# Kernel optimization log

Measured on AMD Instinct MI355X. Metric: run time of the kernel, lower is better.

Reference implementation:

```python
import jax, jax.numpy as jnp
import numpy as np

L, H, P = 16384, 1024, 512
DT_MIN, DT_MAX = 1e-3, 1e-1
STEP_RESCALE = 1.0


def setup_inputs() -> dict:
    key = jax.random.key(0)
    ks = jax.random.split(key, 7)
    input_sequence = jax.random.normal(ks[0], (L, H), jnp.float32)
    # eigenvalues with negative real part (left half plane), HiPPO-like imag parts
    Lambda_re = -(jax.random.uniform(ks[1], (P,), jnp.float32) * 0.9 + 0.1)
    Lambda_im = jnp.pi * jnp.arange(P, dtype=jnp.float32)
    B = jax.random.normal(ks[2], (P, H, 2), jnp.float32) / jnp.sqrt(2.0 * H)   # real/imag of B_tilde (P,H)
    C = jax.random.normal(ks[3], (H, P, 2), jnp.float32) / jnp.sqrt(2.0 * P)   # real/imag of C_tilde (H,P)
    D = jax.random.normal(ks[4], (H,), jnp.float32)
    u01 = jax.random.uniform(ks[5], (P, 1), jnp.float32)
    log_step = jnp.log(DT_MIN) + u01 * (jnp.log(DT_MAX) - jnp.log(DT_MIN))     # (P,1)
    return dict(input_sequence=input_sequence, Lambda_re=Lambda_re, Lambda_im=Lambda_im,
                B=B, C=C, D=D, log_step=log_step)


def _binop(q_i, q_j):
    # diagonal linear recurrence composition: (A, b) pairs
    A_i, b_i = q_i
    A_j, b_j = q_j
    return A_j * A_i, A_j * b_i + b_j


def reference(input_sequence, Lambda_re, Lambda_im, B, C, D, log_step):
    Lambda = Lambda_re + 1j * Lambda_im                        # (P,) complex64
    B_tilde = B[..., 0] + 1j * B[..., 1]                       # (P,H)
    C_tilde = C[..., 0] + 1j * C[..., 1]                       # (H,P)
    step = STEP_RESCALE * jnp.exp(log_step[:, 0])              # (P,)
    # ZOH discretization
    Lambda_bar = jnp.exp(Lambda * step)                        # (P,)
    B_bar = ((Lambda_bar - 1.0) / Lambda)[:, None] * B_tilde   # (P,H)
    # Bu_elements: (L,P) complex
    Bu = input_sequence.astype(B_bar.dtype) @ B_bar.T
    Lambda_elems = jnp.broadcast_to(Lambda_bar, Bu.shape)      # (L,P)
    # parallel associative scan over the diagonal recurrence x_t = Lambda_bar*x_{t-1} + Bu_t
    _, xs = jax.lax.associative_scan(_binop, (Lambda_elems, Bu))
    ys = 2.0 * (xs @ C_tilde.T).real                           # conj_sym => factor 2, (L,H)
    return ys + D * input_sequence
```

## Files before the change

### kernel.cpp

```cpp
#include <hip/hip_runtime.h>
#include <math.h>

#define L_SEQ 16384
#define H_DIM 1024
#define P_DIM 512
#define N2P   1024
#define KDIM  1024
#define NKT   16
#define CHUNK 64
#define NCHUNK 256

typedef __attribute__((ext_vector_type(8))) short short8;
typedef __attribute__((ext_vector_type(4))) float f32x4;
typedef __attribute__((address_space(3))) const char* lds3_t;

__device__ __forceinline__ unsigned short f2bf(float f){
    unsigned int u = __float_as_uint(f);
    u = (u + 0x7FFFu + ((u >> 16) & 1u)) >> 16;
    return (unsigned short)u;
}
__device__ __forceinline__ float bf2f(unsigned int lo16){
    return __uint_as_float(lo16 << 16);
}

__global__ void k_prep_lambda(const float* __restrict__ lre, const float* __restrict__ lim,
                              const float* __restrict__ lstep,
                              float* __restrict__ lam, float* __restrict__ coef,
                              float* __restrict__ lpow, float* __restrict__ wtab)
{
    int p = threadIdx.x;
    double step = exp((double)lstep[p]);
    double dr = (double)lre[p], di = (double)lim[p];
    double ar = dr*step, ai = di*step;
    double er = exp(ar);
    double lbr = er*cos(ai), lbi = er*sin(ai);
    lam[2*p] = (float)lbr; lam[2*p+1] = (float)lbi;
    double nr = lbr - 1.0, ni = lbi;
    double d2 = dr*dr + di*di;
    coef[2*p]   = (float)((nr*dr + ni*di)/d2);
    coef[2*p+1] = (float)((ni*dr - nr*di)/d2);
    double pwr = 1.0, pwi = 0.0;
    for (int tt = 63; tt >= 0; --tt){
        wtab[((size_t)tt*P_DIM + p)*2]     = (float)pwr;
        wtab[((size_t)tt*P_DIM + p)*2 + 1] = (float)pwi;
        double t2 = pwr*lbr - pwi*lbi;
        pwi = pwr*lbi + pwi*lbr;
        pwr = t2;
    }
    double xr = lbr, xi = lbi;
    #pragma unroll
    for (int s=0;s<6;s++){ double t = xr*xr - xi*xi; xi = 2.0*xr*xi; xr = t; }
    lpow[2*p] = (float)xr; lpow[2*p+1] = (float)xi;
}

__global__ __launch_bounds__(256)
void k_prep_misc(const float* __restrict__ B, const float* __restrict__ C,
                 const float* __restrict__ coef,
                 unsigned short* __restrict__ BB, unsigned short* __restrict__ CC,
                 const float4* __restrict__ u, unsigned short* __restrict__ u16)
{
    int bid = blockIdx.x;
    if (bid < 2048){
        int i = bid*256 + threadIdx.x;
        int p = i >> 10, h = i & 1023;
        float br = B[2*i], bi = B[2*i+1];
        float cr = coef[2*p], ci = coef[2*p+1];
        BB[(size_t)(2*p)*H_DIM + h]   = f2bf(cr*br - ci*bi);
        BB[(size_t)(2*p+1)*H_DIM + h] = f2bf(cr*bi + ci*br);
    } else if (bid < 4096){
        int i = (bid-2048)*256 + threadIdx.x;
        int h = i >> 9, p = i & 511;
        float cr = C[2*i], ci = C[2*i+1];
        CC[(size_t)h*N2P + 2*p]     = f2bf(2.f*cr);
        CC[(size_t)h*N2P + 2*p + 1] = f2bf(-2.f*ci);
    } else {
        int i = (bid-4096)*256 + threadIdx.x;
        float4 a = u[2*i], b = u[2*i+1];
        union { short8 v; unsigned short s[8]; } r;
        r.s[0]=f2bf(a.x); r.s[1]=f2bf(a.y); r.s[2]=f2bf(a.z); r.s[3]=f2bf(a.w);
        r.s[4]=f2bf(b.x); r.s[5]=f2bf(b.y); r.s[6]=f2bf(b.z); r.s[7]=f2bf(b.w);
        *reinterpret_cast<short8*>(u16 + (size_t)i*8) = r.v;
    }
}

template<int EPI>
__global__ __launch_bounds__(512, 2)
void gemm256(const unsigned short* __restrict__ A, const unsigned short* __restrict__ Bm,
             float* __restrict__ Cf, unsigned short* __restrict__ Cb,
             const float* __restrict__ Dv, const unsigned short* __restrict__ U16,
             const float* __restrict__ wtab, float* __restrict__ aggOut)
{
    __shared__ char lds[131072];
    const int tid  = threadIdx.x;
    const int lane = tid & 63;
    const int wid  = tid >> 6;
    const int wm = wid >> 2, wn = wid & 3;
    const int wg = ((int)blockIdx.x & 7) * 32 + ((int)blockIdx.x >> 3);
    const int tm = wg >> 2, tn = wg & 3;
    const int lr = lane & 15;

    const int scol = ((tid & 7) ^ ((tid >> 3) & 7)) << 3;
    const int srow = tid >> 3;
    const int kc0 = (((lane >> 4)      ^ (lr & 7)) << 4);
    const int kc1 = ((((lane >> 4) | 4) ^ (lr & 7)) << 4);
    const int aSub = wm*16384 + lr*128;
    const int bSub = 32768 + (wn >> 1)*16384 + (wn & 1)*8192 + lr*128;

#define GLOAD(SRC, DST) __builtin_amdgcn_global_load_lds( \
        (const __attribute__((address_space(1))) void*)(SRC), \
        (__attribute__((address_space(3))) void*)(DST), 16, 0, 0)
#define STAGE_A(src_, par_, h_) do{ \
    char* d_ = lds + ((par_)<<16) + (h_)*16384 + tid*16; \
    const unsigned short* s_ = A + (size_t)(tm*256 + (h_)*128 + srow)*KDIM + (size_t)(src_)*64 + scol; \
    GLOAD(s_, d_); GLOAD(s_ + (size_t)64*KDIM, d_ + 8192); }while(0)
#define STAGE_B(src_, par_, h_) do{ \
    char* d_ = lds + ((par_)<<16) + 32768 + (h_)*16384 + tid*16; \
    const unsigned short* s_ = Bm + (size_t)(tn*256 + (h_)*128 + srow)*KDIM + (size_t)(src_)*64 + scol; \
    GLOAD(s_, d_); GLOAD(s_ + (size_t)64*KDIM, d_ + 8192); }while(0)
#define DSR(D, P, IMM) asm volatile("ds_read_b128 %0, %1 offset:" IMM : "=v"(D) : "v"(P))
#define LGKM(N) do{ asm volatile("s_waitcnt lgkmcnt(" #N ")" ::: "memory"); \
                    __builtin_amdgcn_sched_barrier(0); }while(0)
#define VMC0  asm volatile("s_waitcnt vmcnt(0)" ::: "memory")
#define ABAR  asm volatile("s_barrier" ::: "memory")
#define SB0   __builtin_amdgcn_sched_barrier(0)
#define MFMA(a,b,c) __builtin_amdgcn_mfma_f32_16x16x32_bf16(a,b,c,0,0,0)
#define PRIO1 __builtin_amdgcn_s_setprio(1)
#define PRIO0 __builtin_amdgcn_s_setprio(0)

    short8 a1[4], a2[4], bb0[4], bb1[4];
    f32x4 acc[8][4];
    #pragma unroll
    for (int m=0;m<8;m++)
        #pragma unroll
        for (int n=0;n<4;n++) acc[m][n] = (f32x4){0.f,0.f,0.f,0.f};

    STAGE_A(0,0,0); STAGE_A(0,0,1); STAGE_B(0,0,0); STAGE_B(0,0,1);
    VMC0; ABAR;

    #pragma unroll 2
    for (int kt = 0; kt < NKT; ++kt) {
        const int sb   = (kt & 1) << 16;
        const int dpar = (~kt) & 1;
        const int src  = (kt+1 < NKT) ? kt+1 : NKT-1;
        lds3_t pa0 = (lds3_t)(lds + sb + aSub + kc0);
        lds3_t pa1 = (lds3_t)(lds + sb + aSub + kc1);
        lds3_t pb0 = (lds3_t)(lds + sb + bSub + kc0);
        lds3_t pb1 = (lds3_t)(lds + sb + bSub + kc1);

        DSR(a1[0], pa0, "0");    DSR(a1[1], pa0, "2048");
        DSR(a1[2], pa0, "4096"); DSR(a1[3], pa0, "6144");
        DSR(bb0[0], pb0, "0");    DSR(bb0[1], pb0, "2048");
        DSR(bb0[2], pb0, "4096"); DSR(bb0[3], pb0, "6144");
        STAGE_A(src, dpar, 0); STAGE_A(src, dpar, 1);
        DSR(a2[0], pa0, "8192");  DSR(a2[1], pa0, "10240");
        DSR(a2[2], pa0, "12288"); DSR(a2[3], pa0, "14336");
        LGKM(4);
        PRIO1;
        #pragma unroll
        for (int m=0;m<4;m++)
            #pragma unroll
            for (int n=0;n<4;n++) acc[m][n] = MFMA(a1[m], bb0[n], acc[m][n]);
        PRIO0; SB0;
        DSR(a1[0], pa1, "0");    DSR(a1[1], pa1, "2048");
        DSR(a1[2], pa1, "4096"); DSR(a1[3], pa1, "6144");
        DSR(bb1[0], pb1, "0");    DSR(bb1[1], pb1, "2048");
        DSR(bb1[2], pb1, "4096"); DSR(bb1[3], pb1, "6144");
        STAGE_B(src, dpar, 0); STAGE_B(src, dpar, 1);
        LGKM(8);
        PRIO1;
        #pragma unroll
        for (int m=0;m<4;m++)
            #pragma unroll
            for (int n=0;n<4;n++) acc[4+m][n] = MFMA(a2[m], bb0[n], acc[4+m][n]);
        PRIO0; SB0;
        DSR(a2[0], pa1, "8192");  DSR(a2[1], pa1, "10240");
        DSR(a2[2], pa1, "12288"); DSR(a2[3], pa1, "14336");
        LGKM(4);
        PRIO1;
        #pragma unroll
        for (int m=0;m<4;m++)
            #pragma unroll
            for (int n=0;n<4;n++) acc[m][n] = MFMA(a1[m], bb1[n], acc[m][n]);
        PRIO0; SB0;
        LGKM(0);
        PRIO1;
        #pragma unroll
        for (int m=0;m<4;m++)
            #pragma unroll
            for (int n=0;n<4;n++) acc[4+m][n] = MFMA(a2[m], bb1[n], acc[4+m][n]);
        PRIO0; SB0;
        VMC0;
        ABAR;
    }

    if (!EPI){
        const int q = lane >> 4;
        #pragma unroll
        for (int n=0;n<4;n++){
            const int pg = tn*128 + wn*32 + n*8 + (lr >> 1);
            float wr[16], wi[16];
            #pragma unroll
            for (int mm=0;mm<4;mm++)
                #pragma unroll
                for (int j=0;j<4;j++){
                    const float* wp = wtab + ((size_t)(mm*16 + q*4 + j)*P_DIM + pg)*2;
                    wr[mm*4+j] = wp[0]; wi[mm*4+j] = wp[1];
                }
            #pragma unroll
            for (int h=0; h<2; h++){
                float s1 = 0.f, s2 = 0.f;
                #pragma unroll
                for (int mm=0;mm<4;mm++)
                    #pragma unroll
                    for (int j=0;j<4;j++){
                        float x = acc[h*4+mm][n][j];
                        s1 += wr[mm*4+j]*x;
                        s2 += wi[mm*4+j]*x;
                    }
                s1 += __shfl_xor(s1,16); s1 += __shfl_xor(s1,32);
                s2 += __shfl_xor(s2,16); s2 += __shfl_xor(s2,32);
                float s1p = __shfl_xor(s1,1);
                float s2p = __shfl_xor(s2,1);
                if (lane < 16 && !(lr & 1)){
                    int c = 4*tm + 2*wm + h;
                    float* o = aggOut + ((size_t)c*P_DIM + pg)*2;
                    o[0] = s1 - s2p;
                    o[1] = s2 + s1p;
                }
            }
        }
    }

    const int orow0 = tm*256 + wm*128 + (lane>>4)*4;
    const int ocol0 = tn*256 + wn*64 + lr;
    #pragma unroll
    for (int m=0;m<8;m++){
        #pragma unroll
        for (int n=0;n<4;n++){
            int row = orow0 + m*16, col = ocol0 + n*16;
            #pragma unroll
            for (int j=0;j<4;j++){
                size_t idx = (size_t)(row + j)*N2P + col;
                if (EPI) Cf[idx] = acc[m][n][j] + Dv[col]*bf2f(U16[idx]);
                else     Cb[idx] = f2bf(acc[m][n][j]);
            }
        }
    }
#undef GLOAD
#undef STAGE_A
#undef STAGE_B
#undef DSR
#undef LGKM
#undef VMC0
#undef ABAR
#undef SB0
#undef MFMA
#undef PRIO1
#undef PRIO0
}

__global__ __launch_bounds__(256)
void k_scan(float* __restrict__ agg, const float* __restrict__ lpow)
{
    __shared__ float sr[NCHUNK], si[NCHUNK];
    int c = threadIdx.x, p = blockIdx.x;
    float xr = agg[((size_t)c*P_DIM + p)*2];
    float xi = agg[((size_t)c*P_DIM + p)*2 + 1];
    sr[c] = xr; si[c] = xi;
    float wr = lpow[2*p], wi = lpow[2*p+1];
    for (int s=1; s<NCHUNK; s<<=1){
        __syncthreads();
        float ur = 0.f, ui = 0.f;
        if (c >= s){ ur = sr[c-s]; ui = si[c-s]; }
        __syncthreads();
        xr += wr*ur - wi*ui;
        xi += wr*ui + wi*ur;
        sr[c] = xr; si[c] = xi;
        float t = wr*wr - wi*wi; wi = 2.f*wr*wi; wr = t;
    }
    __syncthreads();
    float er = 0.f, ei = 0.f;
    if (c > 0){ er = sr[c-1]; ei = si[c-1]; }
    agg[((size_t)c*P_DIM + p)*2]     = er;
    agg[((size_t)c*P_DIM + p)*2 + 1] = ei;
}

__global__ __launch_bounds__(512)
void k_apply(const unsigned int* __restrict__ Bu, const float* __restrict__ lam,
             const float* __restrict__ xinit, unsigned int* __restrict__ xs)
{
    int p = threadIdx.x, c = blockIdx.x;
    float lrr = lam[2*p], lii = lam[2*p+1];
    float xr = xinit[((size_t)c*P_DIM + p)*2];
    float xi = xinit[((size_t)c*P_DIM + p)*2 + 1];
    const unsigned int* b2 = Bu + (size_t)c*CHUNK*512 + p;
    unsigned int* o = xs + (size_t)c*CHUNK*512 + p;
    #pragma unroll 4
    for (int t=0;t<CHUNK;t++){
        unsigned int b = b2[(size_t)t*512];
        float br = __uint_as_float(b << 16);
        float bi = __uint_as_float(b & 0xffff0000u);
        float tr = lrr*xr - lii*xi + br;
        xi = lrr*xi + lii*xr + bi;
        xr = tr;
        o[(size_t)t*512] = (unsigned int)f2bf(xr) | ((unsigned int)f2bf(xi) << 16);
    }
}

extern "C" void kernel_launch(void* const* d_in, const int* in_sizes, int n_in,
                              void* d_out, int out_size, void* d_ws, size_t ws_size,
                              hipStream_t stream)
{
    const float* u   = (const float*)d_in[0];
    const float* lre = (const float*)d_in[1];
    const float* lim = (const float*)d_in[2];
    const float* B   = (const float*)d_in[3];
    const float* C   = (const float*)d_in[4];
    const float* D   = (const float*)d_in[5];
    const float* ls  = (const float*)d_in[6];
    float* out = (float*)d_out;

    char* w = (char*)d_ws;
    unsigned short* u16  = (unsigned short*)(w + 0);
    unsigned short* xs16 = (unsigned short*)(w + 33554432);
    unsigned short* Bu16 = (unsigned short*)(w + 67108864);
    unsigned short* BB   = (unsigned short*)(w + 100663296);
    unsigned short* CC   = (unsigned short*)(w + 102760448);
    float* lam   = (float*)(w + 104857600);
    float* coef  = (float*)(w + 104861696);
    float* lpow  = (float*)(w + 104865792);
    float* agg   = (float*)(w + 104869888);
    float* wtab  = (float*)(w + 105918464);

    k_prep_lambda<<<1, P_DIM, 0, stream>>>(lre, lim, ls, lam, coef, lpow, wtab);
    k_prep_misc<<<12288, 256, 0, stream>>>(B, C, coef, BB, CC, (const float4*)u, u16);

    gemm256<0><<<256, 512, 0, stream>>>(u16, BB, nullptr, Bu16, nullptr, nullptr,
                                        wtab, agg);

    k_scan<<<P_DIM, NCHUNK, 0, stream>>>(agg, lpow);
    k_apply<<<NCHUNK, P_DIM, 0, stream>>>((const unsigned int*)Bu16, lam, agg,
                                          (unsigned int*)xs16);

    gemm256<1><<<256, 512, 0, stream>>>(xs16, CC, out, nullptr, D, u16,
                                        nullptr, nullptr);
}
```

Baseline: 123.1 us.

## Fuse chunk scan and apply into first GEMM epilogue with decoupled lookback

Removes the separate scan and apply kernels and the bf16 Bu round trip through global memory. The first GEMM now reduces its chunk aggregates per block and publishes them with flags. Each block then spins on its predecessors' flags, combines their aggregates with precomputed Lambda^256 powers, and runs the per-timestep recurrence from LDS-staged fp32 accumulators, writing xs directly. This avoids two launches and a large write and read of Bu. The cost is a serial lookback dependency across blocks, plus a timeout-guarded spin that assumes all 256 blocks are co-resident, and a largely single-wave serial recurrence inside the epilogue.

Measured after the change: 158.8 us. +29.0%, slower.

```diff
diff --git a/kernel.cpp b/kernel.cpp
--- a/kernel.cpp
+++ b/kernel.cpp
@@ -26,7 +26,8 @@
 __global__ void k_prep_lambda(const float* __restrict__ lre, const float* __restrict__ lim,
                               const float* __restrict__ lstep,
                               float* __restrict__ lam, float* __restrict__ coef,
-                              float* __restrict__ lpow, float* __restrict__ wtab)
+                              float* __restrict__ lpow, float* __restrict__ wtab,
+                              float* __restrict__ wpow256)
 {
     int p = threadIdx.x;
     double step = exp((double)lstep[p]);
@@ -51,6 +52,17 @@
     #pragma unroll
     for (int s=0;s<6;s++){ double t = xr*xr - xi*xi; xi = 2.0*xr*xi; xr = t; }
     lpow[2*p] = (float)xr; lpow[2*p+1] = (float)xi;
+    double qr = xr, qi = xi;
+    #pragma unroll
+    for (int s=0;s<2;s++){ double t = qr*qr - qi*qi; qi = 2.0*qr*qi; qr = t; }
+    double wr_ = 1.0, wi_ = 0.0;
+    for (int d=0; d<64; ++d){
+        wpow256[((size_t)d*P_DIM + p)*2]     = (float)wr_;
+        wpow256[((size_t)d*P_DIM + p)*2 + 1] = (float)wi_;
+        double t2 = wr_*qr - wi_*qi;
+        wi_ = wr_*qi + wi_*qr;
+        wr_ = t2;
+    }
 }
 
 __global__ __launch_bounds__(256)
@@ -86,9 +98,12 @@
 template<int EPI>
 __global__ __launch_bounds__(512, 2)
 void gemm256(const unsigned short* __restrict__ A, const unsigned short* __restrict__ Bm,
-             float* __restrict__ Cf, unsigned short* __restrict__ Cb,
-             const float* __restrict__ Dv, const unsigned short* __restrict__ U16,
-             const float* __restrict__ wtab, float* __restrict__ aggOut)
+             float* __restrict__ Cf, const float* __restrict__ Dv,
+             const unsigned short* __restrict__ U16,
+             const float* __restrict__ wtab, const float* __restrict__ wpow256,
+             const float* __restrict__ lam, const float* __restrict__ lpow,
+             unsigned long long* __restrict__ aggBlkG, unsigned int* __restrict__ flagG,
+             unsigned short* __restrict__ xs16O)
 {
     __shared__ char lds[131072];
     const int tid  = threadIdx.x;
@@ -194,55 +209,156 @@
     }
 
     if (!EPI){
-        const int q = lane >> 4;
-        #pragma unroll
-        for (int n=0;n<4;n++){
-            const int pg = tn*128 + wn*32 + n*8 + (lr >> 1);
-            float wr[16], wi[16];
-            #pragma unroll
-            for (int mm=0;mm<4;mm++)
-                #pragma unroll
-                for (int j=0;j<4;j++){
-                    const float* wp = wtab + ((size_t)(mm*16 + q*4 + j)*P_DIM + pg)*2;
-                    wr[mm*4+j] = wp[0]; wi[mm*4+j] = wp[1];
-                }
-            #pragma unroll
-            for (int h=0; h<2; h++){
-                float s1 = 0.f, s2 = 0.f;
+        float* aggL = (float*)lds;
+        float* xinL = (float*)(lds + 4096);
+        float* plnR = (float*)(lds + 8192);
+        float* plnI = (float*)(lds + 8192 + 33024);
+        {
+            const int q = lane >> 4;
+            #pragma unroll
+            for (int n=0;n<4;n++){
+                const int pb = wn*32 + n*8 + (lr >> 1);
+                const int pg = tn*128 + pb;
+                float wr[16], wi[16];
                 #pragma unroll
                 for (int mm=0;mm<4;mm++)
                     #pragma unroll
                     for (int j=0;j<4;j++){
-                        float x = acc[h*4+mm][n][j];
-                        s1 += wr[mm*4+j]*x;
-                        s2 += wi[mm*4+j]*x;
+                        const float* wp = wtab + ((size_t)(mm*16 + q*4 + j)*P_DIM + pg)*2;
+                        wr[mm*4+j] = wp[0]; wi[mm*4+j] = wp[1];
                     }
-                s1 += __shfl_xor(s1,16); s1 += __shfl_xor(s1,32);
-                s2 += __shfl_xor(s2,16); s2 += __shfl_xor(s2,32);
-                float s1p = __shfl_xor(s1,1);
-                float s2p = __shfl_xor(s2,1);
-                if (lane < 16 && !(lr & 1)){
-                    int c = 4*tm + 2*wm + h;
-                    float* o = aggOut + ((size_t)c*P_DIM + pg)*2;
-                    o[0] = s1 - s2p;
-                    o[1] = s2 + s1p;
+                #pragma unroll
+                for (int h=0; h<2; h++){
+                    float s1 = 0.f, s2 = 0.f;
+                    #pragma unroll
+                    for (int mm=0;mm<4;mm++)
+                        #pragma unroll
+                        for (int j=0;j<4;j++){
+                            float x = acc[h*4+mm][n][j];
+                            s1 += wr[mm*4+j]*x;
+                            s2 += wi[mm*4+j]*x;
+                        }
+                    s1 += __shfl_xor(s1,16); s1 += __shfl_xor(s1,32);
+                    s2 += __shfl_xor(s2,16); s2 += __shfl_xor(s2,32);
+                    float s1p = __shfl_xor(s1,1);
+                    float s2p = __shfl_xor(s2,1);
+                    if (lane < 16 && !(lr & 1)){
+                        int cloc = 2*wm + h;
+                        aggL[(cloc*128 + pb)*2]     = s1 - s2p;
+                        aggL[(cloc*128 + pb)*2 + 1] = s2 + s1p;
+                    }
                 }
             }
         }
-    }
-
-    const int orow0 = tm*256 + wm*128 + (lane>>4)*4;
-    const int ocol0 = tn*256 + wn*64 + lr;
-    #pragma unroll
-    for (int m=0;m<8;m++){
-        #pragma unroll
-        for (int n=0;n<4;n++){
-            int row = orow0 + m*16, col = ocol0 + n*16;
-            #pragma unroll
-            for (int j=0;j<4;j++){
-                size_t idx = (size_t)(row + j)*N2P + col;
-                if (EPI) Cf[idx] = acc[m][n][j] + Dv[col]*bf2f(U16[idx]);
-                else     Cb[idx] = f2bf(acc[m][n][j]);
+        asm volatile("s_waitcnt lgkmcnt(0)" ::: "memory");
+        ABAR;
+        if (tid < 128){
+            int p = tid, pg = tn*128 + p;
+            float l64r = lpow[2*pg], l64i = lpow[2*pg+1];
+            float br = aggL[p*2], bi = aggL[p*2+1];
+            #pragma unroll
+            for (int c=1;c<4;c++){
+                float t_ = br*l64r - bi*l64i + aggL[(c*128+p)*2];
+                bi       = br*l64i + bi*l64r + aggL[(c*128+p)*2+1];
+                br = t_;
+            }
+            unsigned long long pk =
+                ((unsigned long long)__float_as_uint(bi) << 32) | __float_as_uint(br);
+            atomicExch(&aggBlkG[((size_t)tn*64 + tm)*128 + p], pk);
+        }
+        VMC0; ABAR;
+        if (tid == 0){
+            __threadfence();
+            atomicExch(&flagG[tn*64 + tm], 1u);
+        }
+        float Xr = 0.f, Xi = 0.f;
+        if (tid < 128 && tm > 0){
+            int p = tid, pg = tn*128 + p;
+            for (int k=0; k<tm; ++k){
+                int guard = 0;
+                while (atomicAdd(&flagG[tn*64 + k], 0u) == 0u)
+                    if (++guard > (1<<24)) break;
+            }
+            __threadfence();
+            const unsigned long long* ab = aggBlkG + (size_t)tn*64*128;
+            for (int k=0; k<tm; ++k){
+                unsigned long long pk = ab[(size_t)k*128 + p];
+                float br = __uint_as_float((unsigned)pk);
+                float bi = __uint_as_float((unsigned)(pk >> 32));
+                const float* wp = wpow256 + ((size_t)(tm-1-k)*P_DIM + pg)*2;
+                Xr += wp[0]*br - wp[1]*bi;
+                Xi += wp[0]*bi + wp[1]*br;
+            }
+        }
+        if (tid < 128){
+            int p = tid, pg = tn*128 + p;
+            float l64r = lpow[2*pg], l64i = lpow[2*pg+1];
+            float xr_ = Xr, xi_ = Xi;
+            xinL[p*2] = xr_; xinL[p*2+1] = xi_;
+            #pragma unroll
+            for (int c=1;c<4;c++){
+                float t_ = xr_*l64r - xi_*l64i + aggL[((c-1)*128+p)*2];
+                xi_      = xr_*l64i + xi_*l64r + aggL[((c-1)*128+p)*2+1];
+                xr_ = t_;
+                xinL[(c*128+p)*2] = xr_; xinL[(c*128+p)*2+1] = xi_;
+            }
+        }
+        unsigned int* xsO = (unsigned int*)xs16O;
+        #pragma unroll 1
+        for (int h=0; h<2; ++h){
+            #pragma unroll 1
+            for (int ph=0; ph<2; ++ph){
+                asm volatile("s_waitcnt lgkmcnt(0)" ::: "memory");
+                ABAR;
+                if (wm == h && (wn >> 1) == ph){
+                    const int ppb = (wn & 1)*32 + (lr >> 1);
+                    float* pl = (lr & 1) ? plnI : plnR;
+                    #pragma unroll
+                    for (int m=0;m<8;m++){
+                        const int rw = m*16 + (lane>>4)*4;
+                        #pragma unroll
+                        for (int n=0;n<4;n++){
+                            float* d = pl + (ppb + n*8)*129 + rw;
+                            d[0]=acc[m][n][0]; d[1]=acc[m][n][1];
+                            d[2]=acc[m][n][2]; d[3]=acc[m][n][3];
+                        }
+                    }
+                }
+                asm volatile("s_waitcnt lgkmcnt(0)" ::: "memory");
+                ABAR;
+                if (tid < 128){
+                    const int pp = tid & 63, cc = tid >> 6;
+                    const int pg = tn*128 + ph*64 + pp;
+                    const float lrr = lam[2*pg], lii = lam[2*pg+1];
+                    const int cloc = 2*h + cc;
+                    float xr_ = xinL[(cloc*128 + ph*64 + pp)*2];
+                    float xi_ = xinL[(cloc*128 + ph*64 + pp)*2 + 1];
+                    const float* pre = plnR + pp*129 + cc*64;
+                    const float* pim = plnI + pp*129 + cc*64;
+                    unsigned int* o = xsO + (size_t)(tm*256 + h*128 + cc*64)*512 + pg;
+                    #pragma unroll 8
+                    for (int t=0;t<64;t++){
+                        float t_ = xr_*lrr - xi_*lii + pre[t];
+                        xi_      = xr_*lii + xi_*lrr + pim[t];
+                        xr_ = t_;
+                        o[(size_t)t*512] = (unsigned)f2bf(xr_) | ((unsigned)f2bf(xi_) << 16);
+                    }
+                }
+            }
+        }
+    } else {
+        const int orow0 = tm*256 + wm*128 + (lane>>4)*4;
+        const int ocol0 = tn*256 + wn*64 + lr;
+        #pragma unroll
+        for (int m=0;m<8;m++){
+            #pragma unroll
+            for (int n=0;n<4;n++){
+                int row = orow0 + m*16, col = ocol0 + n*16;
+                #pragma unroll
+                for (int j=0;j<4;j++){
+                    size_t idx = (size_t)(row + j)*N2P + col;
+                    Cf[idx] = acc[m][n][j] + Dv[col]*bf2f(U16[idx]);
+                }
             }
         }
     }
@@ -259,54 +375,6 @@
 #undef PRIO0
 }
 
-__global__ __launch_bounds__(256)
-void k_scan(float* __restrict__ agg, const float* __restrict__ lpow)
-{
-    __shared__ float sr[NCHUNK], si[NCHUNK];
-    int c = threadIdx.x, p = blockIdx.x;
-    float xr = agg[((size_t)c*P_DIM + p)*2];
-    float xi = agg[((size_t)c*P_DIM + p)*2 + 1];
-    sr[c] = xr; si[c] = xi;
-    float wr = lpow[2*p], wi = lpow[2*p+1];
-    for (int s=1; s<NCHUNK; s<<=1){
-        __syncthreads();
-        float ur = 0.f, ui = 0.f;
-        if (c >= s){ ur = sr[c-s]; ui = si[c-s]; }
-        __syncthreads();
-        xr += wr*ur - wi*ui;
-        xi += wr*ui + wi*ur;
-        sr[c] = xr; si[c] = xi;
-        float t = wr*wr - wi*wi; wi = 2.f*wr*wi; wr = t;
-    }
-    __syncthreads();
-    float er = 0.f, ei = 0.f;
-    if (c > 0){ er = sr[c-1]; ei = si[c-1]; }
-    agg[((size_t)c*P_DIM + p)*2]     = er;
-    agg[((size_t)c*P_DIM + p)*2 + 1] = ei;
-}
-
-__global__ __launch_bounds__(512)
-void k_apply(const unsigned int* __restrict__ Bu, const float* __restrict__ lam,
-             const float* __restrict__ xinit, unsigned int* __restrict__ xs)
-{
-    int p = threadIdx.x, c = blockIdx.x;
-    float lrr = lam[2*p], lii = lam[2*p+1];
-    float xr = xinit[((size_t)c*P_DIM + p)*2];
-    float xi = xinit[((size_t)c*P_DIM + p)*2 + 1];
-    const unsigned int* b2 = Bu + (size_t)c*CHUNK*512 + p;
-    unsigned int* o = xs + (size_t)c*CHUNK*512 + p;
-    #pragma unroll 4
-    for (int t=0;t<CHUNK;t++){
-        unsigned int b = b2[(size_t)t*512];
-        float br = __uint_as_float(b << 16);
-        float bi = __uint_as_float(b & 0xffff0000u);
-        float tr = lrr*xr - lii*xi + br;
-        xi = lrr*xi + lii*xr + bi;
-        xr = tr;
-        o[(size_t)t*512] = (unsigned int)f2bf(xr) | ((unsigned int)f2bf(xi) << 16);
-    }
-}
-
 extern "C" void kernel_launch(void* const* d_in, const int* in_sizes, int n_in,
                               void* d_out, int out_size, void* d_ws, size_t ws_size,
                               hipStream_t stream)
@@ -323,25 +391,24 @@
     char* w = (char*)d_ws;
     unsigned short* u16  = (unsigned short*)(w + 0);
     unsigned short* xs16 = (unsigned short*)(w + 33554432);
-    unsigned short* Bu16 = (unsigned short*)(w + 67108864);
-    unsigned short* BB   = (unsigned short*)(w + 100663296);
-    unsigned short* CC   = (unsigned short*)(w + 102760448);
-    float* lam   = (float*)(w + 104857600);
-    float* coef  = (float*)(w + 104861696);
-    float* lpow  = (float*)(w + 104865792);
-    float* agg   = (float*)(w + 104869888);
-    float* wtab  = (float*)(w + 105918464);
-
-    k_prep_lambda<<<1, P_DIM, 0, stream>>>(lre, lim, ls, lam, coef, lpow, wtab);
+    unsigned short* BB   = (unsigned short*)(w + 67108864);
+    unsigned short* CC   = (unsigned short*)(w + 69206016);
+    float* lam     = (float*)(w + 71303168);
+    float* coef    = (float*)(w + 71307264);
+    float* lpow    = (float*)(w + 71311360);
+    float* wtab    = (float*)(w + 71315456);
+    float* wpow256 = (float*)(w + 71577600);
+    unsigned long long* aggBlk = (unsigned long long*)(w + 71839744);
+    unsigned int* flags = (unsigned int*)(w + 72101888);
+
+    hipMemsetAsync(flags, 0, 1024, stream);
+    k_prep_lambda<<<1, P_DIM, 0, stream>>>(lre, lim, ls, lam, coef, lpow, wtab, wpow256);
     k_prep_misc<<<12288, 256, 0, stream>>>(B, C, coef, BB, CC, (const float4*)u, u16);
 
-    gemm256<0><<<256, 512, 0, stream>>>(u16, BB, nullptr, Bu16, nullptr, nullptr,
-                                        wtab, agg);
-
-    k_scan<<<P_DIM, NCHUNK, 0, stream>>>(agg, lpow);
-    k_apply<<<NCHUNK, P_DIM, 0, stream>>>((const unsigned int*)Bu16, lam, agg,
-                                          (unsigned int*)xs16);
-
-    gemm256<1><<<256, 512, 0, stream>>>(xs16, CC, out, nullptr, D, u16,
-                                        nullptr, nullptr);
-}
+    gemm256<0><<<256, 512, 0, stream>>>(u16, BB, nullptr, nullptr, nullptr,
+                                        wtab, wpow256, lam, lpow, aggBlk, flags, xs16);
+
+    gemm256<1><<<256, 512, 0, stream>>>(xs16, CC, out, D, u16,
+                                        nullptr, nullptr, nullptr, nullptr,
+                                        nullptr, nullptr, nullptr);
+}
```
